# Optimization experiments

Measured on AMD Instinct MI355X. Metric: run time of the kernel, lower is better.

Reference implementation:

```python
import jax, jax.numpy as jnp
import numpy as np

BATCH, SEQ, IN, HID, OUT = 64, 512, 512, 1024, 512


def setup_inputs() -> dict:
    key = jax.random.key(0)
    ks = jax.random.split(key, 7)
    s_ih = 1.0 / np.sqrt(IN)
    s_hh = 1.0 / np.sqrt(HID)
    return {
        "x_sequence": jax.random.normal(ks[0], (BATCH, SEQ, IN), dtype=jnp.float32),
        "W_ih": jax.random.uniform(ks[1], (HID, IN), jnp.float32, -s_ih, s_ih),
        "b_ih": jax.random.uniform(ks[2], (HID,), jnp.float32, -s_ih, s_ih),
        "W_hh": jax.random.uniform(ks[3], (HID, HID), jnp.float32, -s_hh, s_hh),
        "b_hh": jax.random.uniform(ks[4], (HID,), jnp.float32, -s_hh, s_hh),
        "W_ho": jax.random.uniform(ks[5], (OUT, HID), jnp.float32, -s_hh, s_hh),
        "b_ho": jax.random.uniform(ks[6], (OUT,), jnp.float32, -s_hh, s_hh),
    }


def reference(x_sequence, W_ih, b_ih, W_hh, b_hh, W_ho, b_ho):
    # Elman RNN: h_t = tanh(x_t @ W_ih^T + b_ih + h_{t-1} @ W_hh^T + b_hh)
    # Returned output is the projection of the FINAL hidden state only
    # (per-step outputs in the original are detached bookkeeping).
    # Precompute all input projections in one big GEMM: [B,S,H]
    x_proj = jnp.einsum("bsi,hi->bsh", x_sequence, W_ih) + b_ih + b_hh

    def step(h, xp_t):
        h_new = jnp.tanh(xp_t + h @ W_hh.T)
        return h_new, None

    h0 = jnp.zeros((x_sequence.shape[0], W_hh.shape[0]), dtype=x_sequence.dtype)
    h_final, _ = jax.lax.scan(step, h0, jnp.swapaxes(x_proj, 0, 1))  # scan over time
    output = h_final @ W_ho.T + b_ho  # [B, OUT]
    return output
```

## Files before the change

kernel.cpp:

```cpp
#include <hip/hip_runtime.h>
#include <cstdint>
#include <cstddef>

typedef unsigned short ushort_t;
typedef unsigned int uint_t;
typedef unsigned long long u64_t;
typedef __attribute__((ext_vector_type(8))) short frag16;
typedef __attribute__((ext_vector_type(8))) unsigned short u16x8;
typedef __attribute__((ext_vector_type(4))) float f32x4;

#define SEQ   512
#define INF   512
#define HID   1024
#define OUTF  512
#define GROUPS 16
#define BPG    16
#define NB     4
#define RPB    64
#define WSTR   1040
#define SPIN_LIMIT (1 << 18)

__device__ __forceinline__ float b2f(ushort_t u) {
    union { unsigned int i; float f; } v; v.i = ((unsigned int)u) << 16; return v.f;
}
__device__ __forceinline__ ushort_t f2b(float f) {
    unsigned int u = __float_as_uint(f);
    unsigned int r = (u + 0x7fffu + ((u >> 16) & 1u)) >> 16;
    return (ushort_t)r;
}
__device__ __forceinline__ float fast_tanh(float s) {
    const float e = __expf(2.0f * s);
    return 1.0f - 2.0f * __builtin_amdgcn_rcpf(e + 1.0f);
}

__device__ __forceinline__ void lds_barrier() {
    asm volatile("s_waitcnt lgkmcnt(0)" ::: "memory");
    __builtin_amdgcn_sched_barrier(0);
    __builtin_amdgcn_s_barrier();
    __builtin_amdgcn_sched_barrier(0);
}

__device__ __forceinline__ void cvt8_hilo(const float* __restrict__ src, u16x8* hi, u16x8* lo) {
    const float4 x0 = *(const float4*)src;
    const float4 x1 = *(const float4*)(src + 4);
    float xs[8] = {x0.x,x0.y,x0.z,x0.w,x1.x,x1.y,x1.z,x1.w};
    u16x8 h, l;
#pragma unroll
    for (int j = 0; j < 8; ++j) {
        const ushort_t hb = f2b(xs[j]);
        h[j] = hb;
        l[j] = f2b(xs[j] - b2f(hb));
    }
    *hi = h; if (lo) *lo = l;
}
__device__ __forceinline__ u16x8 cvt8_hi(const float* __restrict__ src) {
    const float4 x0 = *(const float4*)src;
    const float4 x1 = *(const float4*)(src + 4);
    float xs[8] = {x0.x,x0.y,x0.z,x0.w,x1.x,x1.y,x1.z,x1.w};
    u16x8 h;
#pragma unroll
    for (int j = 0; j < 8; ++j) h[j] = f2b(xs[j]);
    return h;
}

__global__ __launch_bounds__(256, 2)
void xproj_kernel(const float* __restrict__ X, const float* __restrict__ Wih,
                  const float* __restrict__ bih, const float* __restrict__ bhh,
                  float* __restrict__ XP)
{
    __shared__ ushort_t Ah[128][40];
    __shared__ ushort_t Al[128][40];
    __shared__ ushort_t Bs[128][40];
    const int tid = (int)threadIdx.x;
    const int m0 = (int)blockIdx.x * 128;
    const int n0 = (int)blockIdx.y * 128;
    const int w  = tid >> 6, l = tid & 63;
    const int wm = (w & 1) * 64, wn = (w >> 1) * 64;
    const int lm = l & 15, lg = l >> 4, hk = lg * 8;
    const int sr = tid >> 2, sc = (tid & 3) * 8;

    f32x4 acc[4][4];
#pragma unroll
    for (int a = 0; a < 4; ++a)
#pragma unroll
        for (int b = 0; b < 4; ++b) { acc[a][b][0]=0.f; acc[a][b][1]=0.f; acc[a][b][2]=0.f; acc[a][b][3]=0.f; }

    for (int ko = 0; ko < INF; ko += 32) {
        __syncthreads();
        u16x8 h, lo;
        cvt8_hilo(&X[(size_t)(m0+sr)*INF + ko + sc], &h, &lo);
        *(u16x8*)&Ah[sr][sc] = h;  *(u16x8*)&Al[sr][sc] = lo;
        cvt8_hilo(&X[(size_t)(m0+sr+64)*INF + ko + sc], &h, &lo);
        *(u16x8*)&Ah[sr+64][sc] = h;  *(u16x8*)&Al[sr+64][sc] = lo;
        *(u16x8*)&Bs[sr][sc]    = cvt8_hi(&Wih[(size_t)(n0+sr)*INF + ko + sc]);
        *(u16x8*)&Bs[sr+64][sc] = cvt8_hi(&Wih[(size_t)(n0+sr+64)*INF + ko + sc]);
        __syncthreads();
        frag16 afh[4], afl[4], bf[4];
#pragma unroll
        for (int i = 0; i < 4; ++i) afh[i] = *(const frag16*)&Ah[wm + i*16 + lm][hk];
#pragma unroll
        for (int i = 0; i < 4; ++i) afl[i] = *(const frag16*)&Al[wm + i*16 + lm][hk];
#pragma unroll
        for (int i = 0; i < 4; ++i) bf[i]  = *(const frag16*)&Bs[wn + i*16 + lm][hk];
#pragma unroll
        for (int a = 0; a < 4; ++a)
#pragma unroll
            for (int b = 0; b < 4; ++b) {
                acc[a][b] = __builtin_amdgcn_mfma_f32_16x16x32_bf16(afh[a], bf[b], acc[a][b], 0, 0, 0);
                acc[a][b] = __builtin_amdgcn_mfma_f32_16x16x32_bf16(afl[a], bf[b], acc[a][b], 0, 0, 0);
            }
    }

#pragma unroll
    for (int b = 0; b < 4; ++b) {
        const int n = n0 + wn + b*16 + lm;
        const float bias = bih[n] + bhh[n];
#pragma unroll
        for (int a = 0; a < 4; ++a)
#pragma unroll
            for (int q = 0; q < 4; ++q) {
                const int m = m0 + wm + a*16 + lg*4 + q;
                XP[(size_t)m * HID + n] = acc[a][b][q] + bias;
            }
    }
}

__global__ __launch_bounds__(256, 1)
void rnn_scan_kernel(const float* __restrict__ XP, const float* __restrict__ Whh,
                     u64_t* __restrict__ Hbuf)
{
    __shared__ ushort_t Ws[RPB][WSTR];
    __shared__ ushort_t Hhi[NB][WSTR];
    __shared__ ushort_t Hlo[NB][WSTR];
    __shared__ float    Cred[4][4][4][16];

    const int tid = (int)threadIdx.x;
    const int w = tid >> 6, l = tid & 63;
    const int lm = l & 15, lg = l >> 4;
    const int gid = (int)blockIdx.x >> 4;
    const int r   = (int)blockIdx.x & 15;
    const int b0 = gid * NB;
    const int j0 = r * RPB;

    {
        const int rr = tid >> 2, cq = (tid & 3) * 256;
        const float* src = Whh + (size_t)(j0 + rr) * HID + cq;
#pragma unroll
        for (int i = 0; i < 32; ++i)
            *(u16x8*)&Ws[rr][cq + i*8] = cvt8_hi(&src[i*8]);
    }
    lds_barrier();

    float xpv[4];
    if (lg == 0) {
#pragma unroll
        for (int q = 0; q < 4; ++q)
            xpv[q] = XP[(size_t)((b0 + q) * SEQ + 0) * HID + (j0 + w*16 + lm)];
    }

    u64_t v[16];

    {
        u64_t pk[4];
        if (lg == 0) {
#pragma unroll
            for (int q = 0; q < 4; ++q) {
                const float hv = fast_tanh(xpv[q]);
                const ushort_t hi = f2b(hv);
                const ushort_t lo = f2b(hv - b2f(hi));
                pk[q] = ((u64_t)((uint_t)hi | ((uint_t)lo << 16)) << 32) | 1ull;
            }
        }
        {
            const u64_t* rown = Hbuf + ((size_t)0 * 64 + b0 + w) * 1024 + l;
#pragma unroll
            for (int j = 0; j < 16; ++j)
                v[j] = __hip_atomic_load(&rown[j*64], __ATOMIC_RELAXED,
                                         __HIP_MEMORY_SCOPE_AGENT);
        }
        if (lg == 0) {
#pragma unroll
            for (int q = 0; q < 4; ++q)
                xpv[q] = XP[(size_t)((b0 + q) * SEQ + 1) * HID + (j0 + w*16 + lm)];
        }
        if (lg == 0) {
            u64_t* outp = Hbuf + ((size_t)0 * 64 + b0) * 1024 + (j0 + w*16 + lm);
#pragma unroll
            for (int q = 0; q < 4; ++q)
                __hip_atomic_store(&outp[(size_t)q * 1024], pk[q],
                                   __ATOMIC_RELAXED, __HIP_MEMORY_SCOPE_AGENT);
        }
    }

    for (int t = 1; t < SEQ; ++t) {
        {
            const u64_t* rowp = Hbuf + ((size_t)((t - 1) & 1) * 64 + b0 + w) * 1024 + l;
            const uint_t want = (uint_t)t;
            int spin = 0;
            for (;;) {
                int bad = 0;
#pragma unroll
                for (int j = 0; j < 16; ++j) bad |= ((uint_t)v[j] != want);
                if (!__any(bad)) break;
                if (++spin > SPIN_LIMIT) break;
                __builtin_amdgcn_s_sleep(1);
#pragma unroll
                for (int j = 0; j < 16; ++j)
                    if ((uint_t)v[j] != want)
                        v[j] = __hip_atomic_load(&rowp[j*64], __ATOMIC_RELAXED,
                                                 __HIP_MEMORY_SCOPE_AGENT);
            }
        }
#pragma unroll
        for (int j = 0; j < 16; ++j) {
            const uint_t d = (uint_t)(v[j] >> 32);
            Hhi[w][l + 64*j] = (ushort_t)(d & 0xffffu);
            Hlo[w][l + 64*j] = (ushort_t)(d >> 16);
        }
        lds_barrier();

        f32x4 acc[4];
#pragma unroll
        for (int i = 0; i < 4; ++i) { acc[i][0]=0.f; acc[i][1]=0.f; acc[i][2]=0.f; acc[i][3]=0.f; }
        {
            const int kbase = w * 256 + lg * 8;
            const ushort_t* ph = &Hhi[lm & 3][kbase];
            const ushort_t* pl = &Hlo[lm & 3][kbase];
            const ushort_t* pw = &Ws[lm][kbase];
#pragma unroll
            for (int kk = 0; kk < 256; kk += 32) {
                const frag16 ahi = *(const frag16*)(ph + kk);
                const frag16 alo = *(const frag16*)(pl + kk);
#pragma unroll
                for (int tl = 0; tl < 4; ++tl) {
                    const frag16 wf = *(const frag16*)(pw + (size_t)tl * 16 * WSTR + kk);
                    acc[tl] = __builtin_amdgcn_mfma_f32_16x16x32_bf16(ahi, wf, acc[tl], 0, 0, 0);
                    acc[tl] = __builtin_amdgcn_mfma_f32_16x16x32_bf16(alo, wf, acc[tl], 0, 0, 0);
                }
            }
        }
        if (lg == 0) {
#pragma unroll
            for (int tl = 0; tl < 4; ++tl)
#pragma unroll
                for (int q = 0; q < 4; ++q)
                    Cred[w][tl][q][lm] = acc[tl][q];
        }
        lds_barrier();

        u64_t pk[4];
        if (lg == 0) {
#pragma unroll
            for (int q = 0; q < 4; ++q) {
                const float s = (Cred[0][w][q][lm] + Cred[1][w][q][lm])
                              + (Cred[2][w][q][lm] + Cred[3][w][q][lm]);
                const float hv = fast_tanh(s + xpv[q]);
                const ushort_t hi = f2b(hv);
                const ushort_t lo = f2b(hv - b2f(hi));
                pk[q] = ((u64_t)((uint_t)hi | ((uint_t)lo << 16)) << 32)
                      | (u64_t)(uint_t)(t + 1);
            }
        }
        if (t + 1 < SEQ) {
            const u64_t* rown = Hbuf + ((size_t)(t & 1) * 64 + b0 + w) * 1024 + l;
#pragma unroll
            for (int j = 0; j < 16; ++j)
                v[j] = __hip_atomic_load(&rown[j*64], __ATOMIC_RELAXED,
                                         __HIP_MEMORY_SCOPE_AGENT);
            if (lg == 0) {
#pragma unroll
                for (int q = 0; q < 4; ++q)
                    xpv[q] = XP[(size_t)((b0 + q) * SEQ + (t + 1)) * HID + (j0 + w*16 + lm)];
            }
        }
        if (lg == 0) {
            u64_t* outp = Hbuf + ((size_t)(t & 1) * 64 + b0) * 1024 + (j0 + w*16 + lm);
#pragma unroll
            for (int q = 0; q < 4; ++q)
                __hip_atomic_store(&outp[(size_t)q * 1024], pk[q],
                                   __ATOMIC_RELAXED, __HIP_MEMORY_SCOPE_AGENT);
        }
    }
}

__global__ __launch_bounds__(256)
void outproj_kernel(const u64_t* __restrict__ Hp, const float* __restrict__ Who,
                    const float* __restrict__ bho, float* __restrict__ Out)
{
    const int tid = (int)threadIdx.x;
    const int w = tid >> 6, l = tid & 63;
    const int lm = l & 15, lg = l >> 4, hk = lg * 8;
    const int n0 = (int)blockIdx.x * 64;

    f32x4 acc[4];
#pragma unroll
    for (int i = 0; i < 4; ++i) { acc[i][0]=0.f; acc[i][1]=0.f; acc[i][2]=0.f; acc[i][3]=0.f; }

    for (int k0 = 0; k0 < HID; k0 += 32) {
        const u64_t* hr = Hp + (size_t)(w*16 + lm) * HID + k0 + hk;
        frag16 ahi, alo;
#pragma unroll
        for (int j = 0; j < 8; ++j) {
            const uint_t d = (uint_t)(hr[j] >> 32);
            ahi[j] = (short)(d & 0xffffu);
            alo[j] = (short)(d >> 16);
        }
#pragma unroll
        for (int bi = 0; bi < 4; ++bi) {
            const u16x8 bv = cvt8_hi(&Who[(size_t)(n0 + bi*16 + lm) * HID + k0 + hk]);
            acc[bi] = __builtin_amdgcn_mfma_f32_16x16x32_bf16(ahi, (frag16)bv, acc[bi], 0, 0, 0);
            acc[bi] = __builtin_amdgcn_mfma_f32_16x16x32_bf16(alo, (frag16)bv, acc[bi], 0, 0, 0);
        }
    }
#pragma unroll
    for (int bi = 0; bi < 4; ++bi) {
        const int n = n0 + bi*16 + lm;
        const float bias = bho[n];
#pragma unroll
        for (int q = 0; q < 4; ++q) {
            const int b = w*16 + lg*4 + q;
            Out[(size_t)b * OUTF + n] = acc[bi][q] + bias;
        }
    }
}

extern "C" void kernel_launch(void* const* d_in, const int* in_sizes, int n_in,
                              void* d_out, int out_size, void* d_ws, size_t ws_size,
                              hipStream_t stream)
{
    const float* X   = (const float*)d_in[0];
    const float* Wih = (const float*)d_in[1];
    const float* bih = (const float*)d_in[2];
    const float* Whh = (const float*)d_in[3];
    const float* bhh = (const float*)d_in[4];
    const float* Who = (const float*)d_in[5];
    const float* bho = (const float*)d_in[6];
    float* Out = (float*)d_out;

    char* ws = (char*)d_ws;
    float* XP = (float*)ws;
    u64_t* Hbuf = (u64_t*)(ws + (size_t)32768 * 1024 * 4);

    xproj_kernel<<<dim3(256, 8), dim3(256), 0, stream>>>(X, Wih, bih, bhh, XP);

    rnn_scan_kernel<<<dim3(GROUPS * BPG), dim3(256), 0, stream>>>(XP, Whh, Hbuf);

    outproj_kernel<<<dim3(OUTF / 64), dim3(256), 0, stream>>>(Hbuf + (size_t)64 * 1024,
                                                              Who, bho, Out);
}
```

Baseline: 2.129 ms.

## Rework RNN scan polling: remap blocks, split H column loads, burn ALU instead of sleep

Remaps block IDs so each group's 16 row-blocks are spread across XCDs or CUs differently. Each wave now polls a 256-column slice of all four batch rows, so it writes only its own K-range of Hhi/Hlo, which removes one LDS barrier per step. Cred is double-buffered by timestep parity. The s_sleep in the spin loop is replaced by dependent FMAC burn sequences with s_setprio toggling, to reduce wake-up latency on the per-step cross-block handoff, at the cost of extra ALU work and power while spinning.

Measured after the change: 2.477 ms. +16.4%, slower.

```diff
diff --git a/kernel.cpp b/kernel.cpp
--- a/kernel.cpp
+++ b/kernel.cpp
@@ -13,8 +13,6 @@
 #define INF   512
 #define HID   1024
 #define OUTF  512
-#define GROUPS 16
-#define BPG    16
 #define NB     4
 #define RPB    64
 #define WSTR   1040
@@ -39,6 +37,17 @@
     __builtin_amdgcn_s_barrier();
     __builtin_amdgcn_sched_barrier(0);
 }
+
+#define BURN16(z0,z1,z2,z3) \
+    asm volatile("v_fmac_f32 %0, %4, %0\n\tv_fmac_f32 %1, %4, %1\n\t"  \
+                 "v_fmac_f32 %2, %4, %2\n\tv_fmac_f32 %3, %4, %3\n\t"  \
+                 "v_fmac_f32 %0, %4, %0\n\tv_fmac_f32 %1, %4, %1\n\t"  \
+                 "v_fmac_f32 %2, %4, %2\n\tv_fmac_f32 %3, %4, %3\n\t"  \
+                 "v_fmac_f32 %0, %4, %0\n\tv_fmac_f32 %1, %4, %1\n\t"  \
+                 "v_fmac_f32 %2, %4, %2\n\tv_fmac_f32 %3, %4, %3\n\t"  \
+                 "v_fmac_f32 %0, %4, %0\n\tv_fmac_f32 %1, %4, %1\n\t"  \
+                 "v_fmac_f32 %2, %4, %2\n\tv_fmac_f32 %3, %4, %3"      \
+                 : "+v"(z0), "+v"(z1), "+v"(z2), "+v"(z3) : "v"(1e-30f))
 
 __device__ __forceinline__ void cvt8_hilo(const float* __restrict__ src, u16x8* hi, u16x8* lo) {
     const float4 x0 = *(const float4*)src;
@@ -132,15 +141,19 @@
     __shared__ ushort_t Ws[RPB][WSTR];
     __shared__ ushort_t Hhi[NB][WSTR];
     __shared__ ushort_t Hlo[NB][WSTR];
-    __shared__ float    Cred[4][4][4][16];
+    __shared__ float    Cred[2][4][4][4][16];
 
     const int tid = (int)threadIdx.x;
     const int w = tid >> 6, l = tid & 63;
     const int lm = l & 15, lg = l >> 4;
-    const int gid = (int)blockIdx.x >> 4;
-    const int r   = (int)blockIdx.x & 15;
+    const int bid = (int)blockIdx.x;
+    const int gid = (bid & 7) * 2 + ((bid >> 3) & 1);
+    const int r   = bid >> 4;
     const int b0 = gid * NB;
     const int j0 = r * RPB;
+    const int qcol = w * 256;
+
+    float z0 = 1.0f + (float)(l & 3), z1 = 2.0f, z2 = 3.0f, z3 = 4.0f;
 
     {
         const int rr = tid >> 2, cq = (tid & 3) * 256;
@@ -150,6 +163,11 @@
             *(u16x8*)&Ws[rr][cq + i*8] = cvt8_hi(&src[i*8]);
     }
     lds_barrier();
+
+    int goff[16];
+#pragma unroll
+    for (int j = 0; j < 16; ++j)
+        goff[j] = (b0 + (j & 3)) * 1024 + qcol + ((j >> 2) << 6) + l;
 
     float xpv[4];
     if (lg == 0) {
@@ -172,10 +190,10 @@
             }
         }
         {
-            const u64_t* rown = Hbuf + ((size_t)0 * 64 + b0 + w) * 1024 + l;
+            const u64_t* base = Hbuf;
 #pragma unroll
             for (int j = 0; j < 16; ++j)
-                v[j] = __hip_atomic_load(&rown[j*64], __ATOMIC_RELAXED,
+                v[j] = __hip_atomic_load(&base[goff[j]], __ATOMIC_RELAXED,
                                          __HIP_MEMORY_SCOPE_AGENT);
         }
         if (lg == 0) {
@@ -184,7 +202,7 @@
                 xpv[q] = XP[(size_t)((b0 + q) * SEQ + 1) * HID + (j0 + w*16 + lm)];
         }
         if (lg == 0) {
-            u64_t* outp = Hbuf + ((size_t)0 * 64 + b0) * 1024 + (j0 + w*16 + lm);
+            u64_t* outp = Hbuf + (size_t)b0 * 1024 + (j0 + w*16 + lm);
 #pragma unroll
             for (int q = 0; q < 4; ++q)
                 __hip_atomic_store(&outp[(size_t)q * 1024], pk[q],
@@ -193,9 +211,14 @@
     }
 
     for (int t = 1; t < SEQ; ++t) {
+        __builtin_amdgcn_s_setprio(0);
         {
-            const u64_t* rowp = Hbuf + ((size_t)((t - 1) & 1) * 64 + b0 + w) * 1024 + l;
+            const u64_t* base = Hbuf + (size_t)((t - 1) & 1) * 65536;
             const uint_t want = (uint_t)t;
+            BURN16(z0,z1,z2,z3); BURN16(z0,z1,z2,z3); BURN16(z0,z1,z2,z3);
+            BURN16(z0,z1,z2,z3); BURN16(z0,z1,z2,z3); BURN16(z0,z1,z2,z3);
+            BURN16(z0,z1,z2,z3); BURN16(z0,z1,z2,z3); BURN16(z0,z1,z2,z3);
+            BURN16(z0,z1,z2,z3); BURN16(z0,z1,z2,z3); BURN16(z0,z1,z2,z3);
             int spin = 0;
             for (;;) {
                 int bad = 0;
@@ -203,27 +226,32 @@
                 for (int j = 0; j < 16; ++j) bad |= ((uint_t)v[j] != want);
                 if (!__any(bad)) break;
                 if (++spin > SPIN_LIMIT) break;
-                __builtin_amdgcn_s_sleep(1);
 #pragma unroll
                 for (int j = 0; j < 16; ++j)
                     if ((uint_t)v[j] != want)
-                        v[j] = __hip_atomic_load(&rowp[j*64], __ATOMIC_RELAXED,
+                        v[j] = __hip_atomic_load(&base[goff[j]], __ATOMIC_RELAXED,
                                                  __HIP_MEMORY_SCOPE_AGENT);
-            }
-        }
+                BURN16(z0,z1,z2,z3); BURN16(z0,z1,z2,z3); BURN16(z0,z1,z2,z3);
+                BURN16(z0,z1,z2,z3); BURN16(z0,z1,z2,z3); BURN16(z0,z1,z2,z3);
+            }
+        }
+        __builtin_amdgcn_s_setprio(1);
+
 #pragma unroll
         for (int j = 0; j < 16; ++j) {
             const uint_t d = (uint_t)(v[j] >> 32);
-            Hhi[w][l + 64*j] = (ushort_t)(d & 0xffffu);
-            Hlo[w][l + 64*j] = (ushort_t)(d >> 16);
-        }
-        lds_barrier();
+            const int c = qcol + ((j >> 2) << 6) + l;
+            Hhi[j & 3][c] = (ushort_t)(d & 0xffffu);
+            Hlo[j & 3][c] = (ushort_t)(d >> 16);
+        }
+        asm volatile("s_waitcnt lgkmcnt(0)" ::: "memory");
+        __builtin_amdgcn_sched_barrier(0);
 
         f32x4 acc[4];
 #pragma unroll
         for (int i = 0; i < 4; ++i) { acc[i][0]=0.f; acc[i][1]=0.f; acc[i][2]=0.f; acc[i][3]=0.f; }
         {
-            const int kbase = w * 256 + lg * 8;
+            const int kbase = qcol + lg * 8;
             const ushort_t* ph = &Hhi[lm & 3][kbase];
             const ushort_t* pl = &Hlo[lm & 3][kbase];
             const ushort_t* pw = &Ws[lm][kbase];
@@ -244,7 +272,7 @@
             for (int tl = 0; tl < 4; ++tl)
 #pragma unroll
                 for (int q = 0; q < 4; ++q)
-                    Cred[w][tl][q][lm] = acc[tl][q];
+                    Cred[t & 1][w][tl][q][lm] = acc[tl][q];
         }
         lds_barrier();
 
@@ -252,8 +280,8 @@
         if (lg == 0) {
 #pragma unroll
             for (int q = 0; q < 4; ++q) {
-                const float s = (Cred[0][w][q][lm] + Cred[1][w][q][lm])
-                              + (Cred[2][w][q][lm] + Cred[3][w][q][lm]);
+                const float s = (Cred[t & 1][0][w][q][lm] + Cred[t & 1][1][w][q][lm])
+                              + (Cred[t & 1][2][w][q][lm] + Cred[t & 1][3][w][q][lm]);
                 const float hv = fast_tanh(s + xpv[q]);
                 const ushort_t hi = f2b(hv);
                 const ushort_t lo = f2b(hv - b2f(hi));
@@ -262,10 +290,10 @@
             }
         }
         if (t + 1 < SEQ) {
-            const u64_t* rown = Hbuf + ((size_t)(t & 1) * 64 + b0 + w) * 1024 + l;
+            const u64_t* base = Hbuf + (size_t)(t & 1) * 65536;
 #pragma unroll
             for (int j = 0; j < 16; ++j)
-                v[j] = __hip_atomic_load(&rown[j*64], __ATOMIC_RELAXED,
+                v[j] = __hip_atomic_load(&base[goff[j]], __ATOMIC_RELAXED,
                                          __HIP_MEMORY_SCOPE_AGENT);
             if (lg == 0) {
 #pragma unroll
@@ -281,6 +309,7 @@
                                    __ATOMIC_RELAXED, __HIP_MEMORY_SCOPE_AGENT);
         }
     }
+    asm volatile("" :: "v"(z0), "v"(z1), "v"(z2), "v"(z3));
 }
 
 __global__ __launch_bounds__(256)
@@ -343,7 +372,7 @@
 
     xproj_kernel<<<dim3(256, 8), dim3(256), 0, stream>>>(X, Wih, bih, bhh, XP);
 
-    rnn_scan_kernel<<<dim3(GROUPS * BPG), dim3(256), 0, stream>>>(XP, Whh, Hbuf);
+    rnn_scan_kernel<<<dim3(256), dim3(256), 0, stream>>>(XP, Whh, Hbuf);
 
     outproj_kernel<<<dim3(OUTF / 64), dim3(256), 0, stream>>>(Hbuf + (size_t)64 * 1024,
                                                               Who, bho, Out);
```
